# Optimization experiments

Measured on AMD Instinct MI355X. Metric: run time of the kernel, lower is better.

The kernel has to match this reference:

```python
import jax, jax.numpy as jnp
import numpy as np

B, N, D = 8, 2048, 512
H = 8
DH = D // H          # 64
SR = 2               # sr_ratio
EPS = 1e-5


def setup_inputs() -> dict:
    key = jax.random.key(0)
    ks = jax.random.split(key, 10)
    s = 0.02
    return {
        "x": jax.random.normal(ks[0], (B, N, D), jnp.float32),
        "x_kv": jax.random.normal(ks[1], (B, N, D), jnp.float32),
        "Wq": jax.random.normal(ks[2], (D, D), jnp.float32) * s,
        "bq": jnp.zeros((D,), jnp.float32),
        "Wsr": jax.random.normal(ks[3], (D, D, SR), jnp.float32) * s,  # (out_ch, in_ch, kernel)
        "bsr": jnp.zeros((D,), jnp.float32),
        "gamma": jnp.ones((D,), jnp.float32),
        "beta": jnp.zeros((D,), jnp.float32),
        "Wkv": jax.random.normal(ks[4], (D, 2 * D), jnp.float32) * s,
        "bkv": jnp.zeros((2 * D,), jnp.float32),
        "Wp": jax.random.normal(ks[5], (DH, DH), jnp.float32) * s,
        "bp": jnp.zeros((DH,), jnp.float32),
    }


def reference(x, x_kv, Wq, bq, Wsr, bsr, gamma, beta, Wkv, bkv, Wp, bp):
    b, n, d = x.shape
    # query projection -> (B, N, H, DH)
    q = (x @ Wq + bq).reshape(b, n, H, DH)

    # spatial reduction: Conv1d(kernel=stride=SR) over sequence, then LayerNorm
    # non-overlapping windows -> reshape + einsum
    xk = x_kv.reshape(b, -1, SR, d)                      # (B, Nk/SR, SR, D)
    xk = jnp.einsum('btsi,ois->bto', xk, Wsr) + bsr       # (B, Nk_eff, D)
    mu = xk.mean(-1, keepdims=True)
    var = jnp.mean((xk - mu) ** 2, -1, keepdims=True)
    xk = (xk - mu) * jax.lax.rsqrt(var + EPS) * gamma + beta

    # kv projection: (B, Nk, 2, H, DH) -> (2, B, H, Nk, DH)
    nk = xk.shape[1]
    kv = (xk @ Wkv + bkv).reshape(b, nk, 2, H, DH)
    kv = jnp.transpose(kv, (2, 0, 3, 1, 4))
    k, v = kv[0], kv[1]                                   # (B, H, Nk, DH)

    # faithful reproduction of original permutes/views
    q = jnp.transpose(q, (2, 0, 1, 3)).reshape(b * H, n, DH)      # (H,B,N,d)->(BH,N,d)
    k = jnp.transpose(k, (2, 0, 1, 3)).reshape(b * H, nk, DH)     # (Nk,B,H,d)->(BH,Nk,d)
    v = jnp.transpose(v, (2, 0, 1, 3)).reshape(b * H, nk, DH)

    scale = float(np.sqrt(DH))
    score = jnp.einsum('bnd,bmd->bnm', q, k) / scale
    attn = jax.nn.softmax(score, axis=-1)
    ctx = jnp.einsum('bnm,bmd->bnd', attn, v)
    ctx = ctx @ Wp + bp                                   # per-head proj Linear(DH, DH)

    ctx = ctx.reshape(H, b, n, DH)
    ctx = jnp.transpose(ctx, (1, 2, 0, 3)).reshape(b, n, H * DH)
    return ctx, attn
```

## Files before the change

### kernel.cpp

```cpp
#include <hip/hip_runtime.h>
#include <cstdint>

using f32x4 = __attribute__((ext_vector_type(4))) float;
using s16x8 = __attribute__((ext_vector_type(8))) short;

__device__ __forceinline__ short f2bf(float f) {
    union { float f; uint32_t u; } x{f};
    uint32_t r = (x.u + 0x7fffu + ((x.u >> 16) & 1u)) >> 16;
    return (short)r;
}
__device__ __forceinline__ float bf2f(short s) {
    union { uint32_t u; float f; } x;
    x.u = ((uint32_t)(uint16_t)s) << 16;
    return x.f;
}

#define MFMA16(a, b, c) __builtin_amdgcn_mfma_f32_16x16x32_bf16(a, b, c, 0, 0, 0)

__device__ __forceinline__ void bar_lgkm() {
    asm volatile("s_waitcnt lgkmcnt(0)\n\ts_barrier" ::: "memory");
}

__device__ __forceinline__ void gl_lds16(const void* g, void* l) {
    __builtin_amdgcn_global_load_lds(
        (const __attribute__((address_space(1))) void*)(const void*)g,
        (__attribute__((address_space(3))) void*)l, 16, 0, 0);
}

__global__ __launch_bounds__(256) void prep_w(
    const float* __restrict__ Wq, const float* __restrict__ Wsr,
    const float* __restrict__ Wkv, const float* __restrict__ Wp,
    short* __restrict__ WqT, short* __restrict__ W2T,
    short* __restrict__ WkvT, short* __restrict__ WpT)
{
    int t = blockIdx.x * 256 + threadIdx.x;
    if (t < 262144) {
        int o = t >> 9, k = t & 511;
        WqT[t] = f2bf(Wq[k * 512 + o]);
    } else if (t < 786432) {
        int u = t - 262144;
        int o = u >> 10, kk = u & 1023;
        int s = kk >> 9, i = kk & 511;
        W2T[u] = f2bf(Wsr[o * 1024 + i * 2 + s]);
    } else if (t < 1310720) {
        int u = t - 786432;
        int c = u >> 9, k = u & 511;
        WkvT[u] = f2bf(Wkv[k * 1024 + c]);
    } else if (t < 1314816) {
        int u = t - 1310720;
        int e = u >> 6, dh = u & 63;
        WpT[u] = f2bf(Wp[dh * 64 + e]);
    }
}

__global__ __launch_bounds__(256) void ln_kernel(
    const float* __restrict__ xkf, const float* __restrict__ gamma,
    const float* __restrict__ beta, short* __restrict__ out)
{
    int row = blockIdx.x * 4 + (threadIdx.x >> 6);
    int lane = threadIdx.x & 63;
    const float* p = xkf + (size_t)row * 512 + lane * 8;
    float4 v0 = *(const float4*)p, v1 = *(const float4*)(p + 4);
    float vv[8] = {v0.x, v0.y, v0.z, v0.w, v1.x, v1.y, v1.z, v1.w};
    float s = 0.f, q = 0.f;
#pragma unroll
    for (int j = 0; j < 8; ++j) { s += vv[j]; q += vv[j] * vv[j]; }
#pragma unroll
    for (int m = 1; m < 64; m <<= 1) { s += __shfl_xor(s, m); q += __shfl_xor(q, m); }
    float mean = s * (1.f / 512.f);
    float var  = q * (1.f / 512.f) - mean * mean;
    float rstd = rsqrtf(var + 1e-5f);
    s16x8 o;
#pragma unroll
    for (int j = 0; j < 8; ++j)
        o[j] = f2bf((vv[j] - mean) * rstd * gamma[lane * 8 + j] + beta[lane * 8 + j]);
    *(s16x8*)(out + (size_t)row * 512 + lane * 8) = o;
}

template <int EPI, int AF32>
__global__ __launch_bounds__(256) void gemm_bt(
    const void* __restrict__ Ap, const short* __restrict__ BT,
    const float* __restrict__ bias,
    float* __restrict__ outF, short* __restrict__ outS, short* __restrict__ outS2,
    int M, int N, int K)
{
    __shared__ short As[128 * 32];
    __shared__ short Bs[128 * 32];
    const int tid = threadIdx.x;
    const int wv = tid >> 6, lane = tid & 63;
    const int l15 = lane & 15, lhi = lane >> 4;
    const int wr = wv >> 1, wc = wv & 1;
    const int m0 = blockIdx.y * 128, n0 = blockIdx.x * 128;

    f32x4 acc[4][4] = {};

    const int nk = K >> 5;
    for (int kk = 0; kk < nk; ++kk) {
#pragma unroll
        for (int i = 0; i < 2; ++i) {
            int fo = wv * 2048 + i * 1024 + lane * 16;
            int row = fo >> 6;
            int ks  = (fo & 63) >> 1;
            if constexpr (AF32) {
                const float* src = (const float*)Ap + (size_t)(m0 + row) * K + kk * 32 + ks;
                float4 a0 = *(const float4*)src;
                float4 a1 = *(const float4*)(src + 4);
                s16x8 pk;
                pk[0] = f2bf(a0.x); pk[1] = f2bf(a0.y); pk[2] = f2bf(a0.z); pk[3] = f2bf(a0.w);
                pk[4] = f2bf(a1.x); pk[5] = f2bf(a1.y); pk[6] = f2bf(a1.z); pk[7] = f2bf(a1.w);
                *(s16x8*)((char*)As + fo) = pk;
            } else {
                gl_lds16((const short*)Ap + (size_t)(m0 + row) * K + kk * 32 + ks, (char*)As + fo);
            }
            gl_lds16(BT + (size_t)(n0 + row) * K + kk * 32 + ks, (char*)Bs + fo);
        }
        __syncthreads();
        s16x8 a[4], b[4];
#pragma unroll
        for (int mi = 0; mi < 4; ++mi)
            a[mi] = *(const s16x8*)&As[(wr * 64 + mi * 16 + l15) * 32 + lhi * 8];
#pragma unroll
        for (int ni = 0; ni < 4; ++ni)
            b[ni] = *(const s16x8*)&Bs[(wc * 64 + ni * 16 + l15) * 32 + lhi * 8];
#pragma unroll
        for (int mi = 0; mi < 4; ++mi)
#pragma unroll
            for (int ni = 0; ni < 4; ++ni)
                acc[mi][ni] = MFMA16(a[mi], b[ni], acc[mi][ni]);
        __syncthreads();
    }

#pragma unroll
    for (int mi = 0; mi < 4; ++mi) {
#pragma unroll
        for (int ni = 0; ni < 4; ++ni) {
#pragma unroll
            for (int r = 0; r < 4; ++r) {
                int grow = m0 + wr * 64 + mi * 16 + lhi * 4 + r;
                int gcol = n0 + wc * 64 + ni * 16 + l15;
                float v = acc[mi][ni][r] + bias[gcol];
                if constexpr (EPI == 0) {
                    int h = gcol >> 6, dh = gcol & 63;
                    int bb = grow >> 11, n = grow & 2047;
                    outS[(((size_t)(h * 8 + bb) * 2048 + n) << 6) + dh] = f2bf(v * 0.125f);
                } else if constexpr (EPI == 1) {
                    outF[(size_t)grow * 512 + gcol] = v;
                } else {
                    int kvsel = gcol >> 9, h = (gcol >> 6) & 7, dh = gcol & 63;
                    int bb = grow >> 10, t = grow & 1023;
                    int g2 = t >> 4, m = ((t & 15) << 6) + bb * 8 + h;
                    if (kvsel == 0)
                        outS[(((size_t)g2 * 1024 + m) << 6) + dh] = f2bf(v);
                    else
                        outS2[(((size_t)g2 * 64 + dh) << 10) + m] = f2bf(v);
                }
            }
        }
    }
}

__global__ __launch_bounds__(512, 4) void attn_kernel(
    const short* __restrict__ Qb, const short* __restrict__ Kb,
    const short* __restrict__ VTb, const short* __restrict__ WpT,
    const float* __restrict__ bp,
    float* __restrict__ ctx_out, float* __restrict__ attn_out)
{
    __shared__ __align__(16) char smem[65536];
    __shared__ float sums[8][32];

    const int bid = blockIdx.x;
    const int swz = ((bid & 7) << 9) | (bid >> 3);
    const int g  = swz >> 6;
    const int n0 = (swz & 63) << 5;
    const int tid = threadIdx.x;
    const int wv = tid >> 6, lane = tid & 63;
    const int l15 = lane & 15, lhi = lane >> 4;

    s16x8 qa00, qa01, qa10, qa11;
    {
        size_t qb0 = (((size_t)g * 2048 + n0 + l15) << 6) + lhi * 8;
        size_t qb1 = (((size_t)g * 2048 + n0 + 16 + l15) << 6) + lhi * 8;
        qa00 = *(const s16x8*)&Qb[qb0];
        qa01 = *(const s16x8*)&Qb[qb0 + 32];
        qa10 = *(const s16x8*)&Qb[qb1];
        qa11 = *(const s16x8*)&Qb[qb1 + 32];
    }

    const short* Kg = Kb + ((size_t)g << 16);
    s16x8 kf[4][2];
#pragma unroll
    for (int p = 0; p < 4; ++p) {
        const short* kr = Kg + (((wv * 8 + p) * 16 + l15) << 6) + lhi * 8;
        kf[p][0] = *(const s16x8*)kr;
        kf[p][1] = *(const s16x8*)(kr + 32);
    }
    float ps0[4] = {}, ps1[4] = {};
#pragma unroll
    for (int i = 0; i < 8; ++i) {
        s16x8 k0 = kf[i & 3][0], k1 = kf[i & 3][1];
        if (i < 4) {
            const short* kr = Kg + (((wv * 8 + i + 4) * 16 + l15) << 6) + lhi * 8;
            kf[i][0] = *(const s16x8*)kr;
            kf[i][1] = *(const s16x8*)(kr + 32);
        }
        int mf = wv * 8 + i;
        f32x4 s0 = {0.f, 0.f, 0.f, 0.f};
        s0 = MFMA16(qa00, k0, s0);
        s0 = MFMA16(qa01, k1, s0);
        f32x4 s1 = {0.f, 0.f, 0.f, 0.f};
        s1 = MFMA16(qa10, k0, s1);
        s1 = MFMA16(qa11, k1, s1);
#pragma unroll
        for (int r = 0; r < 4; ++r) {
            float e0 = __expf(s0[r]);
            ps0[r] += e0;
            int row0 = lhi * 4 + r;
            int byte0 = ((row0 << 11) + ((mf * 16 + l15) << 1)) ^ ((row0 & 7) << 4);
            *(short*)(smem + byte0) = f2bf(e0);
            float e1 = __expf(s1[r]);
            ps1[r] += e1;
            int row1 = 16 + lhi * 4 + r;
            int byte1 = ((row1 << 11) + ((mf * 16 + l15) << 1)) ^ ((row1 & 7) << 4);
            *(short*)(smem + byte1) = f2bf(e1);
        }
    }

    const short* Vg = VTb + ((size_t)g << 16);
    s16x8 vb[2][4];
#pragma unroll
    for (int ni = 0; ni < 4; ++ni) {
        vb[0][ni] = *(const s16x8*)&Vg[((ni * 16 + l15) << 10) + wv * 128 + lhi * 8];
        vb[1][ni] = *(const s16x8*)&Vg[((ni * 16 + l15) << 10) + wv * 128 + 32 + lhi * 8];
    }

#pragma unroll
    for (int r = 0; r < 4; ++r) {
        float v0 = ps0[r], v1 = ps1[r];
        v0 += __shfl_xor(v0, 1); v1 += __shfl_xor(v1, 1);
        v0 += __shfl_xor(v0, 2); v1 += __shfl_xor(v1, 2);
        v0 += __shfl_xor(v0, 4); v1 += __shfl_xor(v1, 4);
        v0 += __shfl_xor(v0, 8); v1 += __shfl_xor(v1, 8);
        ps0[r] = v0; ps1[r] = v1;
    }
    if (l15 == 0) {
#pragma unroll
        for (int r = 0; r < 4; ++r) {
            sums[wv][lhi * 4 + r] = ps0[r];
            sums[wv][16 + lhi * 4 + r] = ps1[r];
        }
    }
    bar_lgkm();

    f32x4 ctx0[4] = {}, ctx1[4] = {};
#pragma unroll
    for (int kk = 0; kk < 4; ++kk) {
        int col = wv * 128 + kk * 32 + lhi * 8;
        s16x8 pv[4];
#pragma unroll
        for (int ni = 0; ni < 4; ++ni) pv[ni] = vb[kk & 1][ni];
        if (kk < 2) {
            int ncol = wv * 128 + (kk + 2) * 32 + lhi * 8;
#pragma unroll
            for (int ni = 0; ni < 4; ++ni)
                vb[kk][ni] = *(const s16x8*)&Vg[((ni * 16 + l15) << 10) + ncol];
        }
        int b0 = ((l15 << 11) + (col << 1)) ^ ((l15 & 7) << 4);
        int b1 = (((16 + l15) << 11) + (col << 1)) ^ ((l15 & 7) << 4);
        s16x8 pf0 = *(const s16x8*)(smem + b0);
        s16x8 pf1 = *(const s16x8*)(smem + b1);
#pragma unroll
        for (int ni = 0; ni < 4; ++ni) {
            ctx0[ni] = MFMA16(pf0, pv[ni], ctx0[ni]);
            ctx1[ni] = MFMA16(pf1, pv[ni], ctx1[ni]);
        }
    }
    __builtin_amdgcn_sched_barrier(0);

#pragma unroll
    for (int rr = 0; rr < 4; ++rr) {
        int row = wv * 4 + rr;
        float tot = 0.f;
#pragma unroll
        for (int w = 0; w < 8; ++w) tot += sums[w][row];
        float inv = 1.f / tot;
        float* arow = attn_out + (((size_t)g * 2048 + n0 + row) << 10);
#pragma unroll
        for (int it = 0; it < 2; ++it) {
            int col = it * 512 + lane * 8;
            int byte = ((row << 11) + (col << 1)) ^ ((row & 7) << 4);
            s16x8 p = *(const s16x8*)(smem + byte);
            f32x4 w0 = {bf2f(p[0]) * inv, bf2f(p[1]) * inv, bf2f(p[2]) * inv, bf2f(p[3]) * inv};
            f32x4 w1 = {bf2f(p[4]) * inv, bf2f(p[5]) * inv, bf2f(p[6]) * inv, bf2f(p[7]) * inv};
            __builtin_nontemporal_store(w0, (f32x4*)(arow + col));
            __builtin_nontemporal_store(w1, (f32x4*)(arow + col + 4));
        }
    }

    bar_lgkm();
    float* cx = (float*)smem;
    if (wv >= 4) {
        int q = wv - 4;
#pragma unroll
        for (int ni = 0; ni < 4; ++ni)
#pragma unroll
            for (int r = 0; r < 4; ++r) {
                cx[(q * 32 + lhi * 4 + r) * 68 + ni * 16 + l15] = ctx0[ni][r];
                cx[(q * 32 + 16 + lhi * 4 + r) * 68 + ni * 16 + l15] = ctx1[ni][r];
            }
    }
    bar_lgkm();
    if (wv < 4) {
#pragma unroll
        for (int ni = 0; ni < 4; ++ni)
#pragma unroll
            for (int r = 0; r < 4; ++r) {
                cx[(wv * 32 + lhi * 4 + r) * 68 + ni * 16 + l15] += ctx0[ni][r];
                cx[(wv * 32 + 16 + lhi * 4 + r) * 68 + ni * 16 + l15] += ctx1[ni][r];
            }
    }
    bar_lgkm();

    if (wv < 2) {
        int rbase = wv * 16;
        float tot = 0.f;
#pragma unroll
        for (int w = 0; w < 8; ++w) tot += sums[w][rbase + l15];
        float invq = 1.f / tot;
        s16x8 ca[2];
#pragma unroll
        for (int kk = 0; kk < 2; ++kk)
#pragma unroll
            for (int j = 0; j < 8; ++j) {
                int k = kk * 32 + lhi * 8 + j;
                int ri = (rbase + l15) * 68 + k;
                float v = cx[ri] + cx[2176 + ri] + cx[4352 + ri] + cx[6528 + ri];
                ca[kk][j] = f2bf(v * invq);
            }
        f32x4 acc2[4] = {};
#pragma unroll
        for (int ni = 0; ni < 4; ++ni) {
            s16x8 b0 = *(const s16x8*)&WpT[((ni * 16 + l15) << 6) + lhi * 8];
            s16x8 b1 = *(const s16x8*)&WpT[((ni * 16 + l15) << 6) + 32 + lhi * 8];
            acc2[ni] = MFMA16(ca[0], b0, acc2[ni]);
            acc2[ni] = MFMA16(ca[1], b1, acc2[ni]);
        }
        const int hh = g >> 3, bb = g & 7;
#pragma unroll
        for (int ni = 0; ni < 4; ++ni)
#pragma unroll
            for (int r = 0; r < 4; ++r) {
                int n = n0 + rbase + lhi * 4 + r;
                int e2 = ni * 16 + l15;
                ctx_out[((size_t)bb * 2048 + n) * 512 + hh * 64 + e2] = acc2[ni][r] + bp[e2];
            }
    }
}

extern "C" void kernel_launch(void* const* d_in, const int* in_sizes, int n_in,
                              void* d_out, int out_size, void* d_ws, size_t ws_size,
                              hipStream_t stream)
{
    const float* x     = (const float*)d_in[0];
    const float* xkv   = (const float*)d_in[1];
    const float* Wq    = (const float*)d_in[2];
    const float* bq    = (const float*)d_in[3];
    const float* Wsr   = (const float*)d_in[4];
    const float* bsr   = (const float*)d_in[5];
    const float* gamma = (const float*)d_in[6];
    const float* beta  = (const float*)d_in[7];
    const float* Wkv   = (const float*)d_in[8];
    const float* bkv   = (const float*)d_in[9];
    const float* Wp    = (const float*)d_in[10];
    const float* bp    = (const float*)d_in[11];

    float* ctx_out  = (float*)d_out;
    float* attn_out = ctx_out + (size_t)8 * 2048 * 512;

    char* sc = (char*)attn_out;
    float* xkf  = (float*)sc;  sc += (size_t)8192 * 512 * 4;
    short* xkln = (short*)sc;  sc += (size_t)8192 * 512 * 2;
    short* WqT  = (short*)sc;  sc += (size_t)512 * 512 * 2;
    short* W2T  = (short*)sc;  sc += (size_t)512 * 1024 * 2;
    short* WkvT = (short*)sc;  sc += (size_t)1024 * 512 * 2;

    char* ws = (char*)d_ws;
    short* Qb  = (short*)ws;   ws += (size_t)64 * 2048 * 64 * 2;
    short* Kb  = (short*)ws;   ws += (size_t)64 * 1024 * 64 * 2;
    short* VTb = (short*)ws;   ws += (size_t)64 * 64 * 1024 * 2;
    short* WpT = (short*)ws;   ws += (size_t)64 * 64 * 2;

    prep_w<<<5136, 256, 0, stream>>>(Wq, Wsr, Wkv, Wp, WqT, W2T, WkvT, WpT);
    gemm_bt<0, 1><<<dim3(4, 128), 256, 0, stream>>>(x, WqT, bq, nullptr, Qb, nullptr, 16384, 512, 512);
    gemm_bt<1, 1><<<dim3(4, 64), 256, 0, stream>>>(xkv, W2T, bsr, xkf, nullptr, nullptr, 8192, 512, 1024);
    ln_kernel<<<2048, 256, 0, stream>>>(xkf, gamma, beta, xkln);
    gemm_bt<2, 0><<<dim3(8, 64), 256, 0, stream>>>(xkln, WkvT, bkv, nullptr, Kb, VTb, 8192, 1024, 512);
    attn_kernel<<<4096, 512, 0, stream>>>(Qb, Kb, VTb, WpT, bp, ctx_out, attn_out);
}
```

Measured before the change: 329.5 us.

## Merge Q and conv GEMMs into one launch, tile weight transposes, use exp2

The Q projection and the strided-conv GEMM now run in a single launch so one grid covers both, and the weight-prep kernel uses LDS-tiled transposes with coalesced loads. The Q scale now folds in log2(e) so the softmax can use exp2f in place of __expf. The attention-probability output is written with plain stores in place of nontemporal ones. Together these aim to cut launch count, tail effects and uncoalesced weight reads. Mixing two GEMM sizes in one grid can leave the blocks unbalanced, and dropping nontemporal stores may pollute the cache.

```diff
diff --git a/kernel.cpp b/kernel.cpp
--- a/kernel.cpp
+++ b/kernel.cpp
@@ -27,29 +27,48 @@
         (__attribute__((address_space(3))) void*)l, 16, 0, 0);
 }
 
-__global__ __launch_bounds__(256) void prep_w(
+__global__ __launch_bounds__(256) void prep_all(
     const float* __restrict__ Wq, const float* __restrict__ Wsr,
     const float* __restrict__ Wkv, const float* __restrict__ Wp,
     short* __restrict__ WqT, short* __restrict__ W2T,
     short* __restrict__ WkvT, short* __restrict__ WpT)
 {
-    int t = blockIdx.x * 256 + threadIdx.x;
-    if (t < 262144) {
-        int o = t >> 9, k = t & 511;
-        WqT[t] = f2bf(Wq[k * 512 + o]);
-    } else if (t < 786432) {
-        int u = t - 262144;
-        int o = u >> 10, kk = u & 1023;
-        int s = kk >> 9, i = kk & 511;
-        W2T[u] = f2bf(Wsr[o * 1024 + i * 2 + s]);
-    } else if (t < 1310720) {
-        int u = t - 786432;
-        int c = u >> 9, k = u & 511;
-        WkvT[u] = f2bf(Wkv[k * 1024 + c]);
-    } else if (t < 1314816) {
-        int u = t - 1310720;
-        int e = u >> 6, dh = u & 63;
-        WpT[u] = f2bf(Wp[dh * 64 + e]);
+    const int b = blockIdx.x, tid = threadIdx.x;
+    if (b < 192) {
+        const float* src; short* dst; int K, N, tk, tn;
+        if (b < 64) { src = Wq;  dst = WqT;  K = 512; N = 512;  tk = b >> 3; tn = b & 7; }
+        else { int u = b - 64; src = Wkv; dst = WkvT; K = 512; N = 1024; tk = u >> 4; tn = u & 15; }
+        const int k0 = tk * 64, n0 = tn * 64;
+        __shared__ float t[64][65];
+        const int lr = tid >> 2, lc = (tid & 3) * 16;
+        const float* s = src + (size_t)(k0 + lr) * N + n0 + lc;
+        float4 a0 = *(const float4*)s, a1 = *(const float4*)(s + 4);
+        float4 a2 = *(const float4*)(s + 8), a3 = *(const float4*)(s + 12);
+        *(float4*)&t[lr][lc]      = a0; *(float4*)&t[lr][lc + 4]  = a1;
+        *(float4*)&t[lr][lc + 8]  = a2; *(float4*)&t[lr][lc + 12] = a3;
+        __syncthreads();
+        const int wn = tid >> 2, wk = (tid & 3) * 16;
+        s16x8 o0, o1;
+#pragma unroll
+        for (int j = 0; j < 8; ++j) {
+            o0[j] = f2bf(t[wk + j][wn]);
+            o1[j] = f2bf(t[wk + 8 + j][wn]);
+        }
+        short* d = dst + (size_t)(n0 + wn) * K + k0 + wk;
+        *(s16x8*)d = o0;
+        *(s16x8*)(d + 8) = o1;
+    } else {
+        for (int u = (b - 192) * 256 + tid; u < 524288 + 4096; u += 208 * 256) {
+            if (u < 524288) {
+                int o = u >> 10, kk = u & 1023;
+                int s2 = kk >> 9, i = kk & 511;
+                W2T[u] = f2bf(Wsr[o * 1024 + i * 2 + s2]);
+            } else {
+                int v = u - 524288;
+                int e = v >> 6, dh = v & 63;
+                WpT[v] = f2bf(Wp[dh * 64 + e]);
+            }
+        }
     }
 }
 
@@ -77,12 +96,87 @@
     *(s16x8*)(out + (size_t)row * 512 + lane * 8) = o;
 }
 
-template <int EPI, int AF32>
-__global__ __launch_bounds__(256) void gemm_bt(
-    const void* __restrict__ Ap, const short* __restrict__ BT,
+__global__ __launch_bounds__(256) void gemm_qconv(
+    const float* __restrict__ x, const float* __restrict__ xkv,
+    const short* __restrict__ WqT, const short* __restrict__ W2T,
+    const float* __restrict__ bq, const float* __restrict__ bsr,
+    short* __restrict__ Qb, float* __restrict__ xkf)
+{
+    __shared__ short As[128 * 32];
+    __shared__ short Bs[128 * 32];
+    const int tid = threadIdx.x;
+    const int wv = tid >> 6, lane = tid & 63;
+    const int l15 = lane & 15, lhi = lane >> 4;
+    const int wr = wv >> 1, wc = wv & 1;
+
+    const int bid = blockIdx.x;
+    const bool isQ = bid < 512;
+    const int u = isQ ? bid : bid - 512;
+    const int m0 = (u >> 2) * 128, n0 = (u & 3) * 128;
+    const int K = isQ ? 512 : 1024;
+    const float* A = isQ ? x : xkv;
+    const short* BT = isQ ? WqT : W2T;
+    const float* bias = isQ ? bq : bsr;
+
+    f32x4 acc[4][4] = {};
+
+    const int nk = K >> 5;
+    for (int kk = 0; kk < nk; ++kk) {
+#pragma unroll
+        for (int i = 0; i < 2; ++i) {
+            int fo = wv * 2048 + i * 1024 + lane * 16;
+            int row = fo >> 6;
+            int ks  = (fo & 63) >> 1;
+            const float* src = A + (size_t)(m0 + row) * K + kk * 32 + ks;
+            float4 a0 = *(const float4*)src;
+            float4 a1 = *(const float4*)(src + 4);
+            s16x8 pk;
+            pk[0] = f2bf(a0.x); pk[1] = f2bf(a0.y); pk[2] = f2bf(a0.z); pk[3] = f2bf(a0.w);
+            pk[4] = f2bf(a1.x); pk[5] = f2bf(a1.y); pk[6] = f2bf(a1.z); pk[7] = f2bf(a1.w);
+            *(s16x8*)((char*)As + fo) = pk;
+            gl_lds16(BT + (size_t)(n0 + row) * K + kk * 32 + ks, (char*)Bs + fo);
+        }
+        __syncthreads();
+        s16x8 a[4], b[4];
+#pragma unroll
+        for (int mi = 0; mi < 4; ++mi)
+            a[mi] = *(const s16x8*)&As[(wr * 64 + mi * 16 + l15) * 32 + lhi * 8];
+#pragma unroll
+        for (int ni = 0; ni < 4; ++ni)
+            b[ni] = *(const s16x8*)&Bs[(wc * 64 + ni * 16 + l15) * 32 + lhi * 8];
+#pragma unroll
+        for (int mi = 0; mi < 4; ++mi)
+#pragma unroll
+            for (int ni = 0; ni < 4; ++ni)
+                acc[mi][ni] = MFMA16(a[mi], b[ni], acc[mi][ni]);
+        __syncthreads();
+    }
+
+#pragma unroll
+    for (int mi = 0; mi < 4; ++mi) {
+#pragma unroll
+        for (int ni = 0; ni < 4; ++ni) {
+#pragma unroll
+            for (int r = 0; r < 4; ++r) {
+                int grow = m0 + wr * 64 + mi * 16 + lhi * 4 + r;
+                int gcol = n0 + wc * 64 + ni * 16 + l15;
+                float v = acc[mi][ni][r] + bias[gcol];
+                if (isQ) {
+                    int h = gcol >> 6, dh = gcol & 63;
+                    int bb = grow >> 11, n = grow & 2047;
+                    Qb[(((size_t)(h * 8 + bb) * 2048 + n) << 6) + dh] = f2bf(v * 0.18033688f);
+                } else {
+                    xkf[(size_t)grow * 512 + gcol] = v;
+                }
+            }
+        }
+    }
+}
+
+__global__ __launch_bounds__(256) void gemm_kv(
+    const short* __restrict__ A, const short* __restrict__ BT,
     const float* __restrict__ bias,
-    float* __restrict__ outF, short* __restrict__ outS, short* __restrict__ outS2,
-    int M, int N, int K)
+    short* __restrict__ Kb, short* __restrict__ VTb, int M, int N, int K)
 {
     __shared__ short As[128 * 32];
     __shared__ short Bs[128 * 32];
@@ -101,17 +195,7 @@
             int fo = wv * 2048 + i * 1024 + lane * 16;
             int row = fo >> 6;
             int ks  = (fo & 63) >> 1;
-            if constexpr (AF32) {
-                const float* src = (const float*)Ap + (size_t)(m0 + row) * K + kk * 32 + ks;
-                float4 a0 = *(const float4*)src;
-                float4 a1 = *(const float4*)(src + 4);
-                s16x8 pk;
-                pk[0] = f2bf(a0.x); pk[1] = f2bf(a0.y); pk[2] = f2bf(a0.z); pk[3] = f2bf(a0.w);
-                pk[4] = f2bf(a1.x); pk[5] = f2bf(a1.y); pk[6] = f2bf(a1.z); pk[7] = f2bf(a1.w);
-                *(s16x8*)((char*)As + fo) = pk;
-            } else {
-                gl_lds16((const short*)Ap + (size_t)(m0 + row) * K + kk * 32 + ks, (char*)As + fo);
-            }
+            gl_lds16(A + (size_t)(m0 + row) * K + kk * 32 + ks, (char*)As + fo);
             gl_lds16(BT + (size_t)(n0 + row) * K + kk * 32 + ks, (char*)Bs + fo);
         }
         __syncthreads();
@@ -139,21 +223,13 @@
                 int grow = m0 + wr * 64 + mi * 16 + lhi * 4 + r;
                 int gcol = n0 + wc * 64 + ni * 16 + l15;
                 float v = acc[mi][ni][r] + bias[gcol];
-                if constexpr (EPI == 0) {
-                    int h = gcol >> 6, dh = gcol & 63;
-                    int bb = grow >> 11, n = grow & 2047;
-                    outS[(((size_t)(h * 8 + bb) * 2048 + n) << 6) + dh] = f2bf(v * 0.125f);
-                } else if constexpr (EPI == 1) {
-                    outF[(size_t)grow * 512 + gcol] = v;
-                } else {
-                    int kvsel = gcol >> 9, h = (gcol >> 6) & 7, dh = gcol & 63;
-                    int bb = grow >> 10, t = grow & 1023;
-                    int g2 = t >> 4, m = ((t & 15) << 6) + bb * 8 + h;
-                    if (kvsel == 0)
-                        outS[(((size_t)g2 * 1024 + m) << 6) + dh] = f2bf(v);
-                    else
-                        outS2[(((size_t)g2 * 64 + dh) << 10) + m] = f2bf(v);
-                }
+                int kvsel = gcol >> 9, h = (gcol >> 6) & 7, dh = gcol & 63;
+                int bb = grow >> 10, t = grow & 1023;
+                int g2 = t >> 4, m = ((t & 15) << 6) + bb * 8 + h;
+                if (kvsel == 0)
+                    Kb[(((size_t)g2 * 1024 + m) << 6) + dh] = f2bf(v);
+                else
+                    VTb[(((size_t)g2 * 64 + dh) << 10) + m] = f2bf(v);
             }
         }
     }
@@ -212,12 +288,12 @@
         s1 = MFMA16(qa11, k1, s1);
 #pragma unroll
         for (int r = 0; r < 4; ++r) {
-            float e0 = __expf(s0[r]);
+            float e0 = exp2f(s0[r]);
             ps0[r] += e0;
             int row0 = lhi * 4 + r;
             int byte0 = ((row0 << 11) + ((mf * 16 + l15) << 1)) ^ ((row0 & 7) << 4);
             *(short*)(smem + byte0) = f2bf(e0);
-            float e1 = __expf(s1[r]);
+            float e1 = exp2f(s1[r]);
             ps1[r] += e1;
             int row1 = 16 + lhi * 4 + r;
             int byte1 = ((row1 << 11) + ((mf * 16 + l15) << 1)) ^ ((row1 & 7) << 4);
@@ -291,8 +367,8 @@
             s16x8 p = *(const s16x8*)(smem + byte);
             f32x4 w0 = {bf2f(p[0]) * inv, bf2f(p[1]) * inv, bf2f(p[2]) * inv, bf2f(p[3]) * inv};
             f32x4 w1 = {bf2f(p[4]) * inv, bf2f(p[5]) * inv, bf2f(p[6]) * inv, bf2f(p[7]) * inv};
-            __builtin_nontemporal_store(w0, (f32x4*)(arow + col));
-            __builtin_nontemporal_store(w1, (f32x4*)(arow + col + 4));
+            *(f32x4*)(arow + col)     = w0;
+            *(f32x4*)(arow + col + 4) = w1;
         }
     }
 
@@ -389,10 +465,9 @@
     short* VTb = (short*)ws;   ws += (size_t)64 * 64 * 1024 * 2;
     short* WpT = (short*)ws;   ws += (size_t)64 * 64 * 2;
 
-    prep_w<<<5136, 256, 0, stream>>>(Wq, Wsr, Wkv, Wp, WqT, W2T, WkvT, WpT);
-    gemm_bt<0, 1><<<dim3(4, 128), 256, 0, stream>>>(x, WqT, bq, nullptr, Qb, nullptr, 16384, 512, 512);
-    gemm_bt<1, 1><<<dim3(4, 64), 256, 0, stream>>>(xkv, W2T, bsr, xkf, nullptr, nullptr, 8192, 512, 1024);
+    prep_all<<<400, 256, 0, stream>>>(Wq, Wsr, Wkv, Wp, WqT, W2T, WkvT, WpT);
+    gemm_qconv<<<768, 256, 0, stream>>>(x, xkv, WqT, W2T, bq, bsr, Qb, xkf);
     ln_kernel<<<2048, 256, 0, stream>>>(xkf, gamma, beta, xkln);
-    gemm_bt<2, 0><<<dim3(8, 64), 256, 0, stream>>>(xkln, WkvT, bkv, nullptr, Kb, VTb, 8192, 1024, 512);
+    gemm_kv<<<dim3(8, 64), 256, 0, stream>>>(xkln, WkvT, bkv, Kb, VTb, 8192, 1024, 512);
     attn_kernel<<<4096, 512, 0, stream>>>(Qb, Kb, VTb, WpT, bp, ctx_out, attn_out);
 }
```

Measured after the change: 344.6 us. 4.6% more time.
